# Kernel tuning notes

Measured on AMD Instinct MI355X. Metric: run time of the kernel, lower is better.

## Reference

```python
import jax, jax.numpy as jnp
import numpy as np

B, H, T, DH = 1, 16, 2048, 64
D = 64  # neighbors per query


def setup_inputs() -> dict:
    key = jax.random.key(0)
    k1, k2, k3, k4, k5, k6 = jax.random.split(key, 6)
    q = jax.random.normal(k1, (B, H, T, DH), dtype=jnp.float32)
    k = jax.random.normal(k2, (B, H, T, DH), dtype=jnp.float32)
    v = jax.random.normal(k3, (B, H, T, DH), dtype=jnp.float32)
    edge_type_bias = jax.random.normal(k4, (4,), dtype=jnp.float32) * 0.1
    neigh_idx = jax.random.randint(k5, (B, H, T, D), 0, T, dtype=jnp.int32)
    edge_type = jax.random.randint(k6, (B, H, T, D), 0, 5, dtype=jnp.int32)
    return {"q": q, "k": k, "v": v, "edge_type_bias": edge_type_bias,
            "neigh_idx": neigh_idx, "edge_type": edge_type}


def _gather_neighbors(x, idx):
    # x: [B,H,T,dh], idx: [B,H,T,D] -> [B,H,T,D,dh]
    return jax.vmap(jax.vmap(lambda xs, ii: xs[ii]))(x, idx)


def reference(q, k, v, edge_type_bias, neigh_idx, edge_type):
    b, h, t, dh = q.shape
    # safe_neighbor_idx: clamp out-of-range indices for the gather
    safe_idx = jnp.clip(neigh_idx, 0, t - 1)
    # causal_neighbor_mask: neighbor j valid iff 0 <= j <= i (original order)
    pos = jnp.arange(t, dtype=neigh_idx.dtype)[None, None, :, None]
    mask = (neigh_idx >= 0) & (neigh_idx <= pos)  # [B,H,T,D]
    k_g = _gather_neighbors(k, safe_idx)  # [B,H,T,D,dh]
    v_g = _gather_neighbors(v, safe_idx)  # [B,H,T,D,dh]
    scores = jnp.einsum('bhte,bhtde->bhtd', q, k_g) / jnp.sqrt(jnp.float32(dh))
    # edge-type bias: table [0, bias0..bias3] indexed by edge_type in {0..4}
    full_bias = jnp.concatenate([jnp.zeros((1,), jnp.float32), edge_type_bias])
    scores = scores + full_bias[edge_type]
    # stable masked softmax (fully-masked rows -> all-zero weights)
    neg = jnp.finfo(scores.dtype).min
    s = jnp.where(mask, scores, neg)
    m = jnp.max(s, axis=-1, keepdims=True)
    e = jnp.exp(s - m) * mask.astype(scores.dtype)
    denom = jnp.sum(e, axis=-1, keepdims=True)
    weights = e / jnp.maximum(denom, 1e-20)
    out = jnp.einsum('bhtd,bhtde->bhte', weights, v_g).astype(v.dtype)
    return out
```

## Files before the change

kernel.cpp:

```cpp
#include <hip/hip_runtime.h>
#include <math.h>


#define T_DIM 2048
#define DH    64
#define NB    64
#define WPB   4

__global__ __launch_bounds__(WPB * 64)
void wayfinder_attn(const float* __restrict__ q,
                    const float* __restrict__ k,
                    const float* __restrict__ v,
                    const float* __restrict__ etb,
                    const int*   __restrict__ neigh_idx,
                    const int*   __restrict__ edge_type,
                    float*       __restrict__ out)
{
    __shared__ int   j_s[WPB][NB];
    __shared__ float b_s[WPB][NB];
    __shared__ float w_s[WPB][NB];
    __shared__ float dot_s[WPB][NB];

    const int lane = threadIdx.x & 63;
    const int wave = threadIdx.x >> 6;

    const int bid = blockIdx.x;
    const int swz = (bid & 7) * 1024 + (bid >> 3);

    const int wq   = swz * WPB + wave;
    const int t    = wq & (T_DIM - 1);
    const int qbase    = wq * DH;
    const int headbase = (wq - t) * DH;
    const float* __restrict__ kh = k + headbase;
    const float* __restrict__ vh = v + headbase;

    j_s[wave][lane] = 0;
    b_s[wave][lane] = 0.f;

    const int raw = neigh_idx[wq * NB + lane];
    const int et  = edge_type[wq * NB + lane];
    const bool valid = (raw >= 0) && (raw <= t);
    const int  sj    = min(max(raw, 0), T_DIM - 1);
    const float bias = (et != 0) ? etb[et - 1] : 0.f;

    const unsigned long long vb = __ballot(valid);
    const int nv  = __popcll(vb);
    const int pos = __popcll(vb & ((1ull << lane) - 1ull));
    if (valid) { j_s[wave][pos] = sj; b_s[wave][pos] = bias; }

    const int c8 = lane & 7;
    const int g8 = lane >> 3;
    const float4 qv0 = *(const float4*)(q + qbase + c8 * 8);
    const float4 qv1 = *(const float4*)(q + qbase + c8 * 8 + 4);

    float4 kr0[8], kr1[8];
    #pragma unroll
    for (int i = 0; i < 8; ++i) {
        if (i * 8 < nv) {
            const int je = j_s[wave][i * 8 + g8];
            kr0[i] = *(const float4*)(kh + je * DH + c8 * 8);
            kr1[i] = *(const float4*)(kh + je * DH + c8 * 8 + 4);
        }
    }

    #pragma unroll
    for (int i = 0; i < 8; ++i) {
        if (i * 8 < nv) {
            float p = kr0[i].x * qv0.x + kr0[i].y * qv0.y
                    + kr0[i].z * qv0.z + kr0[i].w * qv0.w
                    + kr1[i].x * qv1.x + kr1[i].y * qv1.y
                    + kr1[i].z * qv1.z + kr1[i].w * qv1.w;
            p += __shfl_xor(p, 1, 64);
            p += __shfl_xor(p, 2, 64);
            p += __shfl_xor(p, 4, 64);
            if (c8 == 0) dot_s[wave][i * 8 + g8] = p;
        }
    }
    const float mydot = dot_s[wave][lane];

    const bool dval = lane < nv;
    const float score = dval ? (mydot * 0.125f + b_s[wave][lane]) : -INFINITY;
    float m = score;
    #pragma unroll
    for (int o = 32; o > 0; o >>= 1) m = fmaxf(m, __shfl_xor(m, o, 64));
    const float e = dval ? __expf(score - m) : 0.f;
    float s = e;
    #pragma unroll
    for (int o = 32; o > 0; o >>= 1) s += __shfl_xor(s, o, 64);
    const float w = e / fmaxf(s, 1e-20f);
    w_s[wave][lane] = w;

    const int qw   = lane >> 4;
    const int lp16 = lane & 15;
    float4 vr[16];
    #pragma unroll
    for (int i = 0; i < 4; ++i) {
        if (i * 16 < nv) {
            const int4 jd = *(const int4*)&j_s[wave][i * 16 + qw * 4];
            vr[i * 4 + 0] = *(const float4*)(vh + jd.x * DH + lp16 * 4);
            vr[i * 4 + 1] = *(const float4*)(vh + jd.y * DH + lp16 * 4);
            vr[i * 4 + 2] = *(const float4*)(vh + jd.z * DH + lp16 * 4);
            vr[i * 4 + 3] = *(const float4*)(vh + jd.w * DH + lp16 * 4);
        }
    }
    float a0 = 0.f, a1 = 0.f, a2 = 0.f, a3 = 0.f;
    #pragma unroll
    for (int i = 0; i < 4; ++i) {
        if (i * 16 < nv) {
            const float4 wd = *(const float4*)&w_s[wave][i * 16 + qw * 4];
            a0 += wd.x * vr[i * 4 + 0].x;  a1 += wd.x * vr[i * 4 + 0].y;
            a2 += wd.x * vr[i * 4 + 0].z;  a3 += wd.x * vr[i * 4 + 0].w;
            a0 += wd.y * vr[i * 4 + 1].x;  a1 += wd.y * vr[i * 4 + 1].y;
            a2 += wd.y * vr[i * 4 + 1].z;  a3 += wd.y * vr[i * 4 + 1].w;
            a0 += wd.z * vr[i * 4 + 2].x;  a1 += wd.z * vr[i * 4 + 2].y;
            a2 += wd.z * vr[i * 4 + 2].z;  a3 += wd.z * vr[i * 4 + 2].w;
            a0 += wd.w * vr[i * 4 + 3].x;  a1 += wd.w * vr[i * 4 + 3].y;
            a2 += wd.w * vr[i * 4 + 3].z;  a3 += wd.w * vr[i * 4 + 3].w;
        }
    }
    a0 += __shfl_xor(a0, 16, 64);  a1 += __shfl_xor(a1, 16, 64);
    a2 += __shfl_xor(a2, 16, 64);  a3 += __shfl_xor(a3, 16, 64);
    a0 += __shfl_xor(a0, 32, 64);  a1 += __shfl_xor(a1, 32, 64);
    a2 += __shfl_xor(a2, 32, 64);  a3 += __shfl_xor(a3, 32, 64);
    if (lane < 16) {
        float4 o; o.x = a0; o.y = a1; o.z = a2; o.w = a3;
        *(float4*)(out + qbase + lane * 4) = o;
    }
}

extern "C" void kernel_launch(void* const* d_in, const int* in_sizes, int n_in,
                              void* d_out, int out_size, void* d_ws, size_t ws_size,
                              hipStream_t stream)
{
    const float* q   = (const float*)d_in[0];
    const float* k   = (const float*)d_in[1];
    const float* v   = (const float*)d_in[2];
    const float* etb = (const float*)d_in[3];
    const int* neigh_idx = (const int*)d_in[4];
    const int* edge_type = (const int*)d_in[5];
    float* out = (float*)d_out;

    (void)d_ws; (void)ws_size;

    const int total_queries = 16 * T_DIM;
    const int blocks = total_queries / WPB;
    hipLaunchKernelGGL(wayfinder_attn, dim3(blocks), dim3(WPB * 64),
                       0, stream, q, k, v, etb, neigh_idx, edge_type, out);
}
```

Before: 114.7 us.

## Process two queries per wave and chunk K/V gathers for interleaved loads

```diff
diff --git a/kernel.cpp b/kernel.cpp
--- a/kernel.cpp
+++ b/kernel.cpp
@@ -6,8 +6,9 @@
 #define DH    64
 #define NB    64
 #define WPB   4
+#define QPW   2
 
-__global__ __launch_bounds__(WPB * 64)
+__global__ __launch_bounds__(WPB * 64, 3)
 void wayfinder_attn(const float* __restrict__ q,
                     const float* __restrict__ k,
                     const float* __restrict__ v,
@@ -16,115 +17,152 @@
                     const int*   __restrict__ edge_type,
                     float*       __restrict__ out)
 {
-    __shared__ int   j_s[WPB][NB];
-    __shared__ float b_s[WPB][NB];
-    __shared__ float w_s[WPB][NB];
-    __shared__ float dot_s[WPB][NB];
+    __shared__ int   j_s[WPB][QPW][NB];
+    __shared__ float b_s[WPB][QPW][NB];
+    __shared__ float w_s[WPB][QPW][NB];
+    __shared__ float dot_s[WPB][QPW][NB];
 
     const int lane = threadIdx.x & 63;
     const int wave = threadIdx.x >> 6;
 
     const int bid = blockIdx.x;
-    const int swz = (bid & 7) * 1024 + (bid >> 3);
+    const int swz = (bid & 7) * 512 + (bid >> 3);
 
-    const int wq   = swz * WPB + wave;
-    const int t    = wq & (T_DIM - 1);
-    const int qbase    = wq * DH;
-    const int headbase = (wq - t) * DH;
+    const int wqb = (swz * WPB + wave) * QPW;
+
+    int nv[QPW];
+    #pragma unroll
+    for (int qi = 0; qi < QPW; ++qi) {
+        const int wq = wqb + qi;
+        const int t  = wq & (T_DIM - 1);
+        j_s[wave][qi][lane] = 0;
+        b_s[wave][qi][lane] = 0.f;
+        const int raw = neigh_idx[wq * NB + lane];
+        const int et  = edge_type[wq * NB + lane];
+        const bool valid = (raw >= 0) && (raw <= t);
+        const int  sj    = min(max(raw, 0), T_DIM - 1);
+        const float bias = (et != 0) ? etb[et - 1] : 0.f;
+        const unsigned long long vb = __ballot(valid);
+        nv[qi] = __popcll(vb);
+        const int pos = __popcll(vb & ((1ull << lane) - 1ull));
+        if (valid) { j_s[wave][qi][pos] = sj; b_s[wave][qi][pos] = bias; }
+    }
+
+    const int headbase = (wqb - (wqb & (T_DIM - 1))) * DH;
     const float* __restrict__ kh = k + headbase;
     const float* __restrict__ vh = v + headbase;
 
-    j_s[wave][lane] = 0;
-    b_s[wave][lane] = 0.f;
-
-    const int raw = neigh_idx[wq * NB + lane];
-    const int et  = edge_type[wq * NB + lane];
-    const bool valid = (raw >= 0) && (raw <= t);
-    const int  sj    = min(max(raw, 0), T_DIM - 1);
-    const float bias = (et != 0) ? etb[et - 1] : 0.f;
-
-    const unsigned long long vb = __ballot(valid);
-    const int nv  = __popcll(vb);
-    const int pos = __popcll(vb & ((1ull << lane) - 1ull));
-    if (valid) { j_s[wave][pos] = sj; b_s[wave][pos] = bias; }
-
     const int c8 = lane & 7;
     const int g8 = lane >> 3;
-    const float4 qv0 = *(const float4*)(q + qbase + c8 * 8);
-    const float4 qv1 = *(const float4*)(q + qbase + c8 * 8 + 4);
+    float4 qv0[QPW], qv1[QPW];
+    #pragma unroll
+    for (int qi = 0; qi < QPW; ++qi) {
+        qv0[qi] = *(const float4*)(q + (wqb + qi) * DH + c8 * 8);
+        qv1[qi] = *(const float4*)(q + (wqb + qi) * DH + c8 * 8 + 4);
+    }
 
-    float4 kr0[8], kr1[8];
     #pragma unroll
-    for (int i = 0; i < 8; ++i) {
-        if (i * 8 < nv) {
-            const int je = j_s[wave][i * 8 + g8];
-            kr0[i] = *(const float4*)(kh + je * DH + c8 * 8);
-            kr1[i] = *(const float4*)(kh + je * DH + c8 * 8 + 4);
+    for (int c = 0; c < 2; ++c) {
+        float4 kr0[QPW][4], kr1[QPW][4];
+        #pragma unroll
+        for (int qi = 0; qi < QPW; ++qi) {
+            #pragma unroll
+            for (int ii = 0; ii < 4; ++ii) {
+                const int i = c * 4 + ii;
+                if (i * 8 < nv[qi]) {
+                    const int je = j_s[wave][qi][i * 8 + g8];
+                    kr0[qi][ii] = *(const float4*)(kh + je * DH + c8 * 8);
+                    kr1[qi][ii] = *(const float4*)(kh + je * DH + c8 * 8 + 4);
+                }
+            }
+        }
+        #pragma unroll
+        for (int qi = 0; qi < QPW; ++qi) {
+            #pragma unroll
+            for (int ii = 0; ii < 4; ++ii) {
+                const int i = c * 4 + ii;
+                if (i * 8 < nv[qi]) {
+                    float p = kr0[qi][ii].x * qv0[qi].x + kr0[qi][ii].y * qv0[qi].y
+                            + kr0[qi][ii].z * qv0[qi].z + kr0[qi][ii].w * qv0[qi].w
+                            + kr1[qi][ii].x * qv1[qi].x + kr1[qi][ii].y * qv1[qi].y
+                            + kr1[qi][ii].z * qv1[qi].z + kr1[qi][ii].w * qv1[qi].w;
+                    p += __shfl_xor(p, 1, 64);
+                    p += __shfl_xor(p, 2, 64);
+                    p += __shfl_xor(p, 4, 64);
+                    if (c8 == 0) dot_s[wave][qi][i * 8 + g8] = p;
+                }
+            }
         }
     }
 
     #pragma unroll
-    for (int i = 0; i < 8; ++i) {
-        if (i * 8 < nv) {
-            float p = kr0[i].x * qv0.x + kr0[i].y * qv0.y
-                    + kr0[i].z * qv0.z + kr0[i].w * qv0.w
-                    + kr1[i].x * qv1.x + kr1[i].y * qv1.y
-                    + kr1[i].z * qv1.z + kr1[i].w * qv1.w;
-            p += __shfl_xor(p, 1, 64);
-            p += __shfl_xor(p, 2, 64);
-            p += __shfl_xor(p, 4, 64);
-            if (c8 == 0) dot_s[wave][i * 8 + g8] = p;
-        }
+    for (int qi = 0; qi < QPW; ++qi) {
+        const float mydot = dot_s[wave][qi][lane];
+        const bool dval = lane < nv[qi];
+        const float score = dval ? (mydot * 0.125f + b_s[wave][qi][lane]) : -INFINITY;
+        float m = score;
+        #pragma unroll
+        for (int o = 32; o > 0; o >>= 1) m = fmaxf(m, __shfl_xor(m, o, 64));
+        const float e = dval ? __expf(score - m) : 0.f;
+        float s = e;
+        #pragma unroll
+        for (int o = 32; o > 0; o >>= 1) s += __shfl_xor(s, o, 64);
+        w_s[wave][qi][lane] = e / fmaxf(s, 1e-20f);
     }
-    const float mydot = dot_s[wave][lane];
-
-    const bool dval = lane < nv;
-    const float score = dval ? (mydot * 0.125f + b_s[wave][lane]) : -INFINITY;
-    float m = score;
-    #pragma unroll
-    for (int o = 32; o > 0; o >>= 1) m = fmaxf(m, __shfl_xor(m, o, 64));
-    const float e = dval ? __expf(score - m) : 0.f;
-    float s = e;
-    #pragma unroll
-    for (int o = 32; o > 0; o >>= 1) s += __shfl_xor(s, o, 64);
-    const float w = e / fmaxf(s, 1e-20f);
-    w_s[wave][lane] = w;
 
     const int qw   = lane >> 4;
     const int lp16 = lane & 15;
-    float4 vr[16];
+    float a0[QPW] = {0.f, 0.f}, a1[QPW] = {0.f, 0.f};
+    float a2[QPW] = {0.f, 0.f}, a3[QPW] = {0.f, 0.f};
     #pragma unroll
-    for (int i = 0; i < 4; ++i) {
-        if (i * 16 < nv) {
-            const int4 jd = *(const int4*)&j_s[wave][i * 16 + qw * 4];
-            vr[i * 4 + 0] = *(const float4*)(vh + jd.x * DH + lp16 * 4);
-            vr[i * 4 + 1] = *(const float4*)(vh + jd.y * DH + lp16 * 4);
-            vr[i * 4 + 2] = *(const float4*)(vh + jd.z * DH + lp16 * 4);
-            vr[i * 4 + 3] = *(const float4*)(vh + jd.w * DH + lp16 * 4);
+    for (int r = 0; r < 2; ++r) {
+        float4 vr[QPW][2][4];
+        #pragma unroll
+        for (int qi = 0; qi < QPW; ++qi) {
+            #pragma unroll
+            for (int i2 = 0; i2 < 2; ++i2) {
+                const int i = r * 2 + i2;
+                if (i * 16 < nv[qi]) {
+                    const int4 jd = *(const int4*)&j_s[wave][qi][i * 16 + qw * 4];
+                    vr[qi][i2][0] = *(const float4*)(vh + jd.x * DH + lp16 * 4);
+                    vr[qi][i2][1] = *(const float4*)(vh + jd.y * DH + lp16 * 4);
+                    vr[qi][i2][2] = *(const float4*)(vh + jd.z * DH + lp16 * 4);
+                    vr[qi][i2][3] = *(const float4*)(vh + jd.w * DH + lp16 * 4);
+                }
+            }
+        }
+        #pragma unroll
+        for (int qi = 0; qi < QPW; ++qi) {
+            #pragma unroll
+            for (int i2 = 0; i2 < 2; ++i2) {
+                const int i = r * 2 + i2;
+                if (i * 16 < nv[qi]) {
+                    const float4 wd = *(const float4*)&w_s[wave][qi][i * 16 + qw * 4];
+                    a0[qi] += wd.x * vr[qi][i2][0].x;  a1[qi] += wd.x * vr[qi][i2][0].y;
+                    a2[qi] += wd.x * vr[qi][i2][0].z;  a3[qi] += wd.x * vr[qi][i2][0].w;
+                    a0[qi] += wd.y * vr[qi][i2][1].x;  a1[qi] += wd.y * vr[qi][i2][1].y;
+                    a2[qi] += wd.y * vr[qi][i2][1].z;  a3[qi] += wd.y * vr[qi][i2][1].w;
+                    a0[qi] += wd.z * vr[qi][i2][2].x;  a1[qi] += wd.z * vr[qi][i2][2].y;
+                    a2[qi] += wd.z * vr[qi][i2][2].z;  a3[qi] += wd.z * vr[qi][i2][2].w;
+                    a0[qi] += wd.w * vr[qi][i2][3].x;  a1[qi] += wd.w * vr[qi][i2][3].y;
+                    a2[qi] += wd.w * vr[qi][i2][3].z;  a3[qi] += wd.w * vr[qi][i2][3].w;
+                }
+            }
         }
     }
-    float a0 = 0.f, a1 = 0.f, a2 = 0.f, a3 = 0.f;
     #pragma unroll
-    for (int i = 0; i < 4; ++i) {
-        if (i * 16 < nv) {
-            const float4 wd = *(const float4*)&w_s[wave][i * 16 + qw * 4];
-            a0 += wd.x * vr[i * 4 + 0].x;  a1 += wd.x * vr[i * 4 + 0].y;
-            a2 += wd.x * vr[i * 4 + 0].z;  a3 += wd.x * vr[i * 4 + 0].w;
-            a0 += wd.y * vr[i * 4 + 1].x;  a1 += wd.y * vr[i * 4 + 1].y;
-            a2 += wd.y * vr[i * 4 + 1].z;  a3 += wd.y * vr[i * 4 + 1].w;
-            a0 += wd.z * vr[i * 4 + 2].x;  a1 += wd.z * vr[i * 4 + 2].y;
-            a2 += wd.z * vr[i * 4 + 2].z;  a3 += wd.z * vr[i * 4 + 2].w;
-            a0 += wd.w * vr[i * 4 + 3].x;  a1 += wd.w * vr[i * 4 + 3].y;
-            a2 += wd.w * vr[i * 4 + 3].z;  a3 += wd.w * vr[i * 4 + 3].w;
+    for (int qi = 0; qi < QPW; ++qi) {
+        a0[qi] += __shfl_xor(a0[qi], 16, 64);  a1[qi] += __shfl_xor(a1[qi], 16, 64);
+        a2[qi] += __shfl_xor(a2[qi], 16, 64);  a3[qi] += __shfl_xor(a3[qi], 16, 64);
+        a0[qi] += __shfl_xor(a0[qi], 32, 64);  a1[qi] += __shfl_xor(a1[qi], 32, 64);
+        a2[qi] += __shfl_xor(a2[qi], 32, 64);  a3[qi] += __shfl_xor(a3[qi], 32, 64);
+    }
+    if (lane < 16) {
+        #pragma unroll
+        for (int qi = 0; qi < QPW; ++qi) {
+            float4 o; o.x = a0[qi]; o.y = a1[qi]; o.z = a2[qi]; o.w = a3[qi];
+            *(float4*)(out + (wqb + qi) * DH + lane * 4) = o;
         }
-    }
-    a0 += __shfl_xor(a0, 16, 64);  a1 += __shfl_xor(a1, 16, 64);
-    a2 += __shfl_xor(a2, 16, 64);  a3 += __shfl_xor(a3, 16, 64);
-    a0 += __shfl_xor(a0, 32, 64);  a1 += __shfl_xor(a1, 32, 64);
-    a2 += __shfl_xor(a2, 32, 64);  a3 += __shfl_xor(a3, 32, 64);
-    if (lane < 16) {
-        float4 o; o.x = a0; o.y = a1; o.z = a2; o.w = a3;
-        *(float4*)(out + qbase + lane * 4) = o;
     }
 }
 
@@ -143,7 +181,7 @@
     (void)d_ws; (void)ws_size;
 
     const int total_queries = 16 * T_DIM;
-    const int blocks = total_queries / WPB;
+    const int blocks = total_queries / (WPB * QPW);
     hipLaunchKernelGGL(wayfinder_attn, dim3(blocks), dim3(WPB * 64),
                        0, stream, q, k, v, etb, neigh_idx, edge_type, out);
 }
```

After: 120.3 us. 1.05x slower.
